# Kernel optimization log

Hardware: AMD Instinct MI355X
Metric: run time of the kernel (lower is better)

Reference implementation:

```python
import jax, jax.numpy as jnp
import numpy as np

N_REP = 8      # N: repeated gelu(LN(linear)) blocks
M_LAYERS = 4   # M: transformer encoder layers
SEQ = 100
D = 4
FF = 2048      # PyTorch TransformerEncoderLayer default dim_feedforward
H = 4          # nhead; head_dim = 1


def _ln(x, g, b, axes):
    m = jnp.mean(x, axis=axes, keepdims=True)
    v = jnp.var(x, axis=axes, keepdims=True)
    return (x - m) / jnp.sqrt(v + 1e-5) * g + b


def _encoder_layer(x, Win, bi, Wout, bout, W1, b1, W2, b2, g1, be1, g2, be2):
    # x: [S, Nb, D] with S = batch_size (batch_first=False!), Nb = 100
    S, Nb, E = x.shape
    qkv = x @ Win.T + bi                      # [S, Nb, 3D]
    q, k, v = jnp.split(qkv, 3, axis=-1)
    qh = q.reshape(S, Nb, H, E // H)          # head_dim = 1, scale 1/sqrt(1)=1
    kh = k.reshape(S, Nb, H, E // H)
    vh = v.reshape(S, Nb, H, E // H)
    scores = jnp.einsum('snhd,tnhd->nhst', qh, kh)   # [Nb, H, S, S]
    attn = jax.nn.softmax(scores, axis=-1)
    o = jnp.einsum('nhst,tnhd->snhd', attn, vh).reshape(S, Nb, E)
    o = o @ Wout.T + bout
    x = _ln(x + o, g1, be1, (-1,))            # post-norm (norm_first=False)
    f = jax.nn.relu(x @ W1.T + b1) @ W2.T + b2
    return _ln(x + f, g2, be2, (-1,))


def setup_inputs() -> dict:
    key = jax.random.key(0)
    ks = jax.random.split(key, 24)
    B = 256
    d = {}
    d['x'] = jax.random.normal(ks[0], (B, SEQ, D), dtype=jnp.float32)
    # conv1: kernel_size=1, 1->1 channel -> scalar affine
    d['conv_w'] = jax.random.normal(ks[1], (), dtype=jnp.float32) * 0.5 + 1.0
    d['conv_b'] = jax.random.normal(ks[2], (), dtype=jnp.float32) * 0.1
    # shared 4x4 linear (self.liner) and LayerNorm([100,4])
    d['Wl'] = jax.random.normal(ks[3], (D, D), dtype=jnp.float32) * 0.5
    d['bl'] = jax.random.normal(ks[4], (D,), dtype=jnp.float32) * 0.1
    d['ln_g'] = jnp.ones((SEQ, D), dtype=jnp.float32)
    d['ln_b'] = jnp.zeros((SEQ, D), dtype=jnp.float32)
    # transformer encoder params, stacked over M layers
    s = 0.3
    d['Win'] = jax.random.normal(ks[5], (M_LAYERS, 3 * D, D), dtype=jnp.float32) * s
    d['bi'] = jax.random.normal(ks[6], (M_LAYERS, 3 * D), dtype=jnp.float32) * 0.05
    d['Wout'] = jax.random.normal(ks[7], (M_LAYERS, D, D), dtype=jnp.float32) * s
    d['bout'] = jax.random.normal(ks[8], (M_LAYERS, D), dtype=jnp.float32) * 0.05
    d['W1'] = jax.random.normal(ks[9], (M_LAYERS, FF, D), dtype=jnp.float32) * 0.05
    d['b1'] = jax.random.normal(ks[10], (M_LAYERS, FF), dtype=jnp.float32) * 0.05
    d['W2'] = jax.random.normal(ks[11], (M_LAYERS, D, FF), dtype=jnp.float32) * 0.02
    d['b2'] = jax.random.normal(ks[12], (M_LAYERS, D), dtype=jnp.float32) * 0.05
    d['g1'] = jnp.ones((M_LAYERS, D), dtype=jnp.float32)
    d['be1'] = jnp.zeros((M_LAYERS, D), dtype=jnp.float32)
    d['g2'] = jnp.ones((M_LAYERS, D), dtype=jnp.float32)
    d['be2'] = jnp.zeros((M_LAYERS, D), dtype=jnp.float32)
    return d


def reference(x, conv_w, conv_b, Wl, bl, ln_g, ln_b,
              Win, bi, Wout, bout, W1, b1, W2, b2, g1, be1, g2, be2):
    # per-channel kernel_size=1 conv == elementwise affine (same scalar for all 4 channels)
    h = x * conv_w + conv_b                   # [B, 100, 4]
    for _ in range(N_REP):
        h = jax.nn.gelu(_ln(h @ Wl.T + bl, ln_g, ln_b, (-2, -1)), approximate=False)
    h = h @ Wl.T + bl
    for i in range(M_LAYERS):
        h = _encoder_layer(h, Win[i], bi[i], Wout[i], bout[i], W1[i], b1[i],
                           W2[i], b2[i], g1[i], be1[i], g2[i], be2[i])
    h = h @ Wl.T + bl
    return jax.nn.softmax(h, axis=2)
```

## Files before the change

### kernel.cpp

```cpp
#include <hip/hip_runtime.h>
#include <math.h>

#define SEQ   100
#define BATCH 256
#define NREP  8
#define FFD   2048
#define RSQRT2 0.70710678118654752440f

__device__ __forceinline__ float wsum(float v) {
#pragma unroll
  for (int o = 32; o > 0; o >>= 1) v += __shfl_xor(v, o, 64);
  return v;
}

__global__ __launch_bounds__(64) void k_stageA(
    const float* __restrict__ x, const float* __restrict__ convw,
    const float* __restrict__ convb, const float* __restrict__ Wl,
    const float* __restrict__ bl, const float* __restrict__ lng,
    const float* __restrict__ lnb, float* __restrict__ XT)
{
  const int b = blockIdx.x;
  const int lane = threadIdx.x;
  const bool act = lane < 50;

  const float cw = convw[0], cb = convb[0];
  float W[4][4], B[4];
#pragma unroll
  for (int j = 0; j < 4; ++j) {
    B[j] = bl[j];
#pragma unroll
    for (int d = 0; d < 4; ++d) W[j][d] = Wl[j * 4 + d];
  }

  float h[2][4] = {{0.f,0.f,0.f,0.f},{0.f,0.f,0.f,0.f}};
  float gg[2][4] = {{0.f}}, eb[2][4] = {{0.f}};
  if (act) {
#pragma unroll
    for (int p = 0; p < 2; ++p) {
      const int r = lane * 2 + p;
      float4 xr = *(const float4*)(x + (b * SEQ + r) * 4);
      h[p][0] = fmaf(xr.x, cw, cb); h[p][1] = fmaf(xr.y, cw, cb);
      h[p][2] = fmaf(xr.z, cw, cb); h[p][3] = fmaf(xr.w, cw, cb);
      float4 gv = *(const float4*)(lng + r * 4);
      float4 bv = *(const float4*)(lnb + r * 4);
      gg[p][0] = gv.x; gg[p][1] = gv.y; gg[p][2] = gv.z; gg[p][3] = gv.w;
      eb[p][0] = bv.x; eb[p][1] = bv.y; eb[p][2] = bv.z; eb[p][3] = bv.w;
    }
  }
  for (int it = 0; it < NREP; ++it) {
    float y[2][4] = {{0.f,0.f,0.f,0.f},{0.f,0.f,0.f,0.f}};
    float s1 = 0.f, s2 = 0.f;
    if (act) {
#pragma unroll
      for (int p = 0; p < 2; ++p)
#pragma unroll
        for (int j = 0; j < 4; ++j) {
          float yy = B[j];
#pragma unroll
          for (int d = 0; d < 4; ++d) yy = fmaf(h[p][d], W[j][d], yy);
          y[p][j] = yy; s1 += yy; s2 = fmaf(yy, yy, s2);
        }
    }
    s1 = wsum(s1); s2 = wsum(s2);
    const float mean = s1 * (1.0f / 400.0f);
    const float var  = s2 * (1.0f / 400.0f) - mean * mean;
    const float rstd = rsqrtf(var + 1e-5f);
    if (act) {
#pragma unroll
      for (int p = 0; p < 2; ++p)
#pragma unroll
        for (int j = 0; j < 4; ++j) {
          float vv = fmaf((y[p][j] - mean) * rstd, gg[p][j], eb[p][j]);
          h[p][j] = 0.5f * vv * (1.0f + erff(vv * RSQRT2));
        }
    }
  }
  if (act) {
#pragma unroll
    for (int p = 0; p < 2; ++p) {
      const int r = lane * 2 + p;
      float yy[4];
#pragma unroll
      for (int j = 0; j < 4; ++j) {
        float a = B[j];
#pragma unroll
        for (int d = 0; d < 4; ++d) a = fmaf(h[p][d], W[j][d], a);
        yy[j] = a;
      }
      *(float4*)(XT + (r * BATCH + b) * 4) =
          make_float4(yy[0], yy[1], yy[2], yy[3]);
    }
  }
}

__global__ __launch_bounds__(512) void k_layer(
    const float* __restrict__ XTin, float* __restrict__ XTout,
    const float* __restrict__ Wa,  const float* __restrict__ ba,
    const float* __restrict__ Wo,  const float* __restrict__ bo,
    const float* __restrict__ W1l, const float* __restrict__ b1l,
    const float* __restrict__ W2l, const float* __restrict__ b2l,
    const float* __restrict__ g1l, const float* __restrict__ e1l,
    const float* __restrict__ g2l, const float* __restrict__ e2l,
    const float* __restrict__ Wl,  const float* __restrict__ bl,
    float* __restrict__ out, const int last)
{
  const int n      = blockIdx.x;
  const int base_s = blockIdx.y * 128;
  const int t      = threadIdx.x;
  const int lane   = t & 63;
  const int wv     = t >> 6;
  const int h      = t >> 7;
  const int qr     = t & 127;

  __shared__ __align__(16) float wbuf[512][12];
  __shared__ float2 kv[4][256];
  __shared__ float  osm[4][128];
  __shared__ float  x1s[128][4];
  __shared__ float  pacc[8][128][4];
  __shared__ float  kred[8][2];

  float4 s_w1; float s_b1, s_w20, s_w21, s_w22, s_w23;
  {
    const int f = t;
    s_w1  = *(const float4*)(W1l + f * 4);
    s_b1  = b1l[f];
    s_w20 = W2l[f];           s_w21 = W2l[FFD + f];
    s_w22 = W2l[2 * FFD + f]; s_w23 = W2l[3 * FFD + f];
  }

  {
    const int s = t & 255, pr = t >> 8;
    float4 xr = *(const float4*)(XTin + (n * BATCH + s) * 4);
#pragma unroll
    for (int i = 0; i < 2; ++i) {
      const int hh = pr * 2 + i;
      const float* wk = Wa + (4 + hh) * 4;
      const float* wp = Wa + (8 + hh) * 4;
      float k = ba[4+hh] + xr.x*wk[0] + xr.y*wk[1] + xr.z*wk[2] + xr.w*wk[3];
      float v = ba[8+hh] + xr.x*wp[0] + xr.y*wp[1] + xr.z*wp[2] + xr.w*wp[3];
      kv[hh][s] = make_float2(k, v);
    }
  }
  float q;
  {
    float4 xr = *(const float4*)(XTin + (n * BATCH + base_s + qr) * 4);
    const float* wq = Wa + h * 4;
    q = ba[h] + xr.x*wq[0] + xr.y*wq[1] + xr.z*wq[2] + xr.w*wq[3];
  }
  __syncthreads();

  {
    float a = kv[h][qr].x, c = kv[h][qr + 128].x;
    float mx = fmaxf(a, c), mn = fminf(a, c);
#pragma unroll
    for (int o = 32; o > 0; o >>= 1) {
      mx = fmaxf(mx, __shfl_xor(mx, o, 64));
      mn = fminf(mn, __shfl_xor(mn, o, 64));
    }
    if (lane == 0) { kred[wv][0] = mx; kred[wv][1] = mn; }
  }
  __syncthreads();

  {
    const float kmx = fmaxf(kred[2*h][0], kred[2*h+1][0]);
    const float kmn = fminf(kred[2*h][1], kred[2*h+1][1]);
    const float m = (q >= 0.f) ? q * kmx : q * kmn;
    float d0=0.f,d1=0.f,d2=0.f,d3=0.f,n0=0.f,n1=0.f,n2=0.f,n3=0.f;
#pragma unroll 4
    for (int t2 = 0; t2 < 256; t2 += 8) {
      float4 a = *(const float4*)&kv[h][t2];
      float4 b = *(const float4*)&kv[h][t2+2];
      float4 c = *(const float4*)&kv[h][t2+4];
      float4 e = *(const float4*)&kv[h][t2+6];
      float p0 = __expf(fmaf(q, a.x, -m)); d0 += p0; n0 = fmaf(p0, a.y, n0);
      float p1 = __expf(fmaf(q, a.z, -m)); d1 += p1; n1 = fmaf(p1, a.w, n1);
      float p2 = __expf(fmaf(q, b.x, -m)); d2 += p2; n2 = fmaf(p2, b.y, n2);
      float p3 = __expf(fmaf(q, b.z, -m)); d3 += p3; n3 = fmaf(p3, b.w, n3);
      p0 = __expf(fmaf(q, c.x, -m)); d0 += p0; n0 = fmaf(p0, c.y, n0);
      p1 = __expf(fmaf(q, c.z, -m)); d1 += p1; n1 = fmaf(p1, c.w, n1);
      p2 = __expf(fmaf(q, e.x, -m)); d2 += p2; n2 = fmaf(p2, e.y, n2);
      p3 = __expf(fmaf(q, e.z, -m)); d3 += p3; n3 = fmaf(p3, e.w, n3);
    }
    osm[h][qr] = (n0+n1+n2+n3) / (d0+d1+d2+d3);
  }
  __syncthreads();

  {
    const int r = t >> 2, d = t & 3;
    const int g = n * BATCH + base_s + r;
    const float o0 = osm[0][r], o1 = osm[1][r], o2 = osm[2][r], o3 = osm[3][r];
    float rr = XTin[g * 4 + d] + bo[d]
             + o0 * Wo[d*4+0] + o1 * Wo[d*4+1] + o2 * Wo[d*4+2] + o3 * Wo[d*4+3];
    float sum = rr + __shfl_xor(rr, 1, 64); sum += __shfl_xor(sum, 2, 64);
    const float mean = 0.25f * sum;
    const float dv = rr - mean;
    float qq = dv * dv;
    float qs = qq + __shfl_xor(qq, 1, 64); qs += __shfl_xor(qs, 2, 64);
    const float rstd = rsqrtf(0.25f * qs + 1e-5f);
    x1s[r][d] = fmaf(dv * rstd, g1l[d], e1l[d]);
  }
  __syncthreads();

  const float xA0 = x1s[lane][0],    xA1 = x1s[lane][1];
  const float xA2 = x1s[lane][2],    xA3 = x1s[lane][3];
  const float xB0 = x1s[64+lane][0], xB1 = x1s[64+lane][1];
  const float xB2 = x1s[64+lane][2], xB3 = x1s[64+lane][3];
  float aA0=0.f,aA1=0.f,aA2=0.f,aA3=0.f;
  float aB0=0.f,aB1=0.f,aB2=0.f,aB3=0.f;

  for (int p = 0; p < 4; ++p) {
    __syncthreads();
    *(float4*)&wbuf[t][0] = s_w1;
    *(float4*)&wbuf[t][4] = make_float4(s_b1, s_w20, s_w21, s_w22);
    wbuf[t][8] = s_w23;
    if (p < 3) {
      const int f = (p + 1) * 512 + t;
      s_w1  = *(const float4*)(W1l + f * 4);
      s_b1  = b1l[f];
      s_w20 = W2l[f];           s_w21 = W2l[FFD + f];
      s_w22 = W2l[2 * FFD + f]; s_w23 = W2l[3 * FFD + f];
    }
    __syncthreads();
    const int fb = wv * 64;
#pragma unroll 4
    for (int j = 0; j < 64; ++j) {
      const int fl = fb + j;
      const float4 w1 = *(const float4*)&wbuf[fl][0];
      const float4 wb = *(const float4*)&wbuf[fl][4];
      const float w23 = wbuf[fl][8];
      float hA = fmaf(xA3, w1.w, fmaf(xA2, w1.z, fmaf(xA1, w1.y, fmaf(xA0, w1.x, wb.x))));
      hA = fmaxf(hA, 0.f);
      aA0 = fmaf(hA, wb.y, aA0); aA1 = fmaf(hA, wb.z, aA1);
      aA2 = fmaf(hA, wb.w, aA2); aA3 = fmaf(hA, w23, aA3);
      float hB = fmaf(xB3, w1.w, fmaf(xB2, w1.z, fmaf(xB1, w1.y, fmaf(xB0, w1.x, wb.x))));
      hB = fmaxf(hB, 0.f);
      aB0 = fmaf(hB, wb.y, aB0); aB1 = fmaf(hB, wb.z, aB1);
      aB2 = fmaf(hB, wb.w, aB2); aB3 = fmaf(hB, w23, aB3);
    }
  }
  *(float4*)&pacc[wv][lane][0]      = make_float4(aA0, aA1, aA2, aA3);
  *(float4*)&pacc[wv][64 + lane][0] = make_float4(aB0, aB1, aB2, aB3);
  __syncthreads();

  {
    const int r = t >> 2, d = t & 3;
    float s8 = b2l[d];
#pragma unroll
    for (int w = 0; w < 8; ++w) s8 += pacc[w][r][d];
    float val = x1s[r][d] + s8;
    float sum = val + __shfl_xor(val, 1, 64); sum += __shfl_xor(sum, 2, 64);
    const float mean = 0.25f * sum;
    const float dv = val - mean;
    float qq = dv * dv;
    float qs = qq + __shfl_xor(qq, 1, 64); qs += __shfl_xor(qs, 2, 64);
    const float rstd = rsqrtf(0.25f * qs + 1e-5f);
    const float res = fmaf(dv * rstd, g2l[d], e2l[d]);
    if (!last) XTout[(n * BATCH + base_s + r) * 4 + d] = res;
    else       x1s[r][d] = res;
  }

  if (last) {
    __syncthreads();
    const int r = t >> 2, j = t & 3;
    const float y = fmaf(x1s[r][3], Wl[j*4+3], fmaf(x1s[r][2], Wl[j*4+2],
                    fmaf(x1s[r][1], Wl[j*4+1], fmaf(x1s[r][0], Wl[j*4+0], bl[j]))));
    float mx = fmaxf(y, __shfl_xor(y, 1, 64)); mx = fmaxf(mx, __shfl_xor(mx, 2, 64));
    const float e = __expf(y - mx);
    float se = e + __shfl_xor(e, 1, 64); se += __shfl_xor(se, 2, 64);
    out[((base_s + r) * SEQ + n) * 4 + j] = e / se;
  }
}

extern "C" void kernel_launch(void* const* d_in, const int* in_sizes, int n_in,
                              void* d_out, int out_size, void* d_ws, size_t ws_size,
                              hipStream_t stream)
{
  const float* x     = (const float*)d_in[0];
  const float* convw = (const float*)d_in[1];
  const float* convb = (const float*)d_in[2];
  const float* Wl    = (const float*)d_in[3];
  const float* bl    = (const float*)d_in[4];
  const float* lng   = (const float*)d_in[5];
  const float* lnb   = (const float*)d_in[6];
  const float* Win   = (const float*)d_in[7];
  const float* bi    = (const float*)d_in[8];
  const float* Wout  = (const float*)d_in[9];
  const float* bout  = (const float*)d_in[10];
  const float* W1    = (const float*)d_in[11];
  const float* b1    = (const float*)d_in[12];
  const float* W2    = (const float*)d_in[13];
  const float* b2    = (const float*)d_in[14];
  const float* g1    = (const float*)d_in[15];
  const float* be1   = (const float*)d_in[16];
  const float* g2    = (const float*)d_in[17];
  const float* be2   = (const float*)d_in[18];

  float* XT0 = (float*)d_ws;
  float* XT1 = XT0 + SEQ * BATCH * 4;

  k_stageA<<<BATCH, 64, 0, stream>>>(x, convw, convb, Wl, bl, lng, lnb, XT0);
  for (int l = 0; l < 4; ++l) {
    const float* in  = (l & 1) ? XT1 : XT0;
    float*       outb= (l & 1) ? XT0 : XT1;
    k_layer<<<dim3(SEQ, 2), 512, 0, stream>>>(
        in, outb,
        Win + l * 48, bi + l * 12, Wout + l * 16, bout + l * 4,
        W1 + l * FFD * 4, b1 + l * FFD, W2 + l * 4 * FFD, b2 + l * 4,
        g1 + l * 4, be1 + l * 4, g2 + l * 4, be2 + l * 4,
        Wl, bl, (float*)d_out, (l == 3) ? 1 : 0);
  }
}
```

Measured before the change: 121.7 us.

## Split layer grid over FFN halves instead of sequence halves, defer LN2 to next layer

Each layer block now processes all 256 sequence rows but only half of the 2048 FFN features. Attention and LN1 are therefore computed redundantly in both blocks, while each FFN weight is loaded and reused across four row groups per thread. The two half-sum partials are written separately; the next layer (or a new final kernel) adds them and applies LN2. This removes the per-block weight streaming of all 2048 features and adds an extra partial buffer plus duplicated attention work.

```diff
diff --git a/kernel.cpp b/kernel.cpp
--- a/kernel.cpp
+++ b/kernel.cpp
@@ -5,6 +5,7 @@
 #define BATCH 256
 #define NREP  8
 #define FFD   2048
+#define COL   (SEQ * BATCH * 4)
 #define RSQRT2 0.70710678118654752440f
 
 __device__ __forceinline__ float wsum(float v) {
@@ -17,7 +18,7 @@
     const float* __restrict__ x, const float* __restrict__ convw,
     const float* __restrict__ convb, const float* __restrict__ Wl,
     const float* __restrict__ bl, const float* __restrict__ lng,
-    const float* __restrict__ lnb, float* __restrict__ XT)
+    const float* __restrict__ lnb, float* __restrict__ xG)
 {
   const int b = blockIdx.x;
   const int lane = threadIdx.x;
@@ -31,7 +32,6 @@
 #pragma unroll
     for (int d = 0; d < 4; ++d) W[j][d] = Wl[j * 4 + d];
   }
-
   float h[2][4] = {{0.f,0.f,0.f,0.f},{0.f,0.f,0.f,0.f}};
   float gg[2][4] = {{0.f}}, eb[2][4] = {{0.f}};
   if (act) {
@@ -87,70 +87,95 @@
         for (int d = 0; d < 4; ++d) a = fmaf(h[p][d], W[j][d], a);
         yy[j] = a;
       }
-      *(float4*)(XT + (r * BATCH + b) * 4) =
+      *(float4*)(xG + (r * BATCH + b) * 4) =
           make_float4(yy[0], yy[1], yy[2], yy[3]);
     }
   }
 }
 
 __global__ __launch_bounds__(512) void k_layer(
-    const float* __restrict__ XTin, float* __restrict__ XTout,
+    const float* __restrict__ in0, const float* __restrict__ in1,
+    const int first,
+    const float* __restrict__ g2p, const float* __restrict__ e2p,
+    float* __restrict__ vout,
     const float* __restrict__ Wa,  const float* __restrict__ ba,
     const float* __restrict__ Wo,  const float* __restrict__ bo,
     const float* __restrict__ W1l, const float* __restrict__ b1l,
     const float* __restrict__ W2l, const float* __restrict__ b2l,
-    const float* __restrict__ g1l, const float* __restrict__ e1l,
-    const float* __restrict__ g2l, const float* __restrict__ e2l,
-    const float* __restrict__ Wl,  const float* __restrict__ bl,
-    float* __restrict__ out, const int last)
+    const float* __restrict__ g1l, const float* __restrict__ e1l)
 {
-  const int n      = blockIdx.x;
-  const int base_s = blockIdx.y * 128;
-  const int t      = threadIdx.x;
-  const int lane   = t & 63;
-  const int wv     = t >> 6;
-  const int h      = t >> 7;
-  const int qr     = t & 127;
+  const int n    = blockIdx.x;
+  const int fh   = blockIdx.y;
+  const int t    = threadIdx.x;
+  const int lane = t & 63;
+  const int wv   = t >> 6;
+  const int h    = t >> 7;
+  const int qr0  = t & 127;
+  const int qr1  = qr0 + 128;
 
   __shared__ __align__(16) float wbuf[512][12];
   __shared__ float2 kv[4][256];
-  __shared__ float  osm[4][128];
-  __shared__ float  x1s[128][4];
-  __shared__ float  pacc[8][128][4];
+  __shared__ float  xs[256][4];
+  __shared__ float  x1s[256][4];
+  __shared__ float  osm[4][256];
+  __shared__ float  pacc[4][256][4];
   __shared__ float  kred[8][2];
 
+  const int fbase = fh * 1024;
   float4 s_w1; float s_b1, s_w20, s_w21, s_w22, s_w23;
   {
-    const int f = t;
+    const int f = fbase + t;
     s_w1  = *(const float4*)(W1l + f * 4);
     s_b1  = b1l[f];
     s_w20 = W2l[f];           s_w21 = W2l[FFD + f];
     s_w22 = W2l[2 * FFD + f]; s_w23 = W2l[3 * FFD + f];
   }
 
+  if (t < 256) {
+    if (first) {
+      float4 a = *(const float4*)(in0 + (n * BATCH + t) * 4);
+      xs[t][0] = a.x; xs[t][1] = a.y; xs[t][2] = a.z; xs[t][3] = a.w;
+    } else {
+      float4 a = *(const float4*)(in0 + (n * BATCH + t) * 4);
+      float4 b = *(const float4*)(in1 + (n * BATCH + t) * 4);
+      float v0 = a.x + b.x, v1 = a.y + b.y, v2 = a.z + b.z, v3 = a.w + b.w;
+      const float mean = 0.25f * (v0 + v1 + v2 + v3);
+      float d0 = v0-mean, d1 = v1-mean, d2 = v2-mean, d3 = v3-mean;
+      const float var = 0.25f * (d0*d0 + d1*d1 + d2*d2 + d3*d3);
+      const float rstd = rsqrtf(var + 1e-5f);
+      xs[t][0] = fmaf(d0 * rstd, g2p[0], e2p[0]);
+      xs[t][1] = fmaf(d1 * rstd, g2p[1], e2p[1]);
+      xs[t][2] = fmaf(d2 * rstd, g2p[2], e2p[2]);
+      xs[t][3] = fmaf(d3 * rstd, g2p[3], e2p[3]);
+    }
+  }
+  __syncthreads();
+
   {
     const int s = t & 255, pr = t >> 8;
-    float4 xr = *(const float4*)(XTin + (n * BATCH + s) * 4);
+    const float x0 = xs[s][0], x1 = xs[s][1], x2 = xs[s][2], x3 = xs[s][3];
 #pragma unroll
     for (int i = 0; i < 2; ++i) {
       const int hh = pr * 2 + i;
       const float* wk = Wa + (4 + hh) * 4;
       const float* wp = Wa + (8 + hh) * 4;
-      float k = ba[4+hh] + xr.x*wk[0] + xr.y*wk[1] + xr.z*wk[2] + xr.w*wk[3];
-      float v = ba[8+hh] + xr.x*wp[0] + xr.y*wp[1] + xr.z*wp[2] + xr.w*wp[3];
+      float k = ba[4+hh] + x0*wk[0] + x1*wk[1] + x2*wk[2] + x3*wk[3];
+      float v = ba[8+hh] + x0*wp[0] + x1*wp[1] + x2*wp[2] + x3*wp[3];
       kv[hh][s] = make_float2(k, v);
     }
   }
-  float q;
-  {
-    float4 xr = *(const float4*)(XTin + (n * BATCH + base_s + qr) * 4);
+  float q0, q1;
+  {
     const float* wq = Wa + h * 4;
-    q = ba[h] + xr.x*wq[0] + xr.y*wq[1] + xr.z*wq[2] + xr.w*wq[3];
-  }
-  __syncthreads();
-
-  {
-    float a = kv[h][qr].x, c = kv[h][qr + 128].x;
+    q0 = ba[h] + xs[qr0][0]*wq[0] + xs[qr0][1]*wq[1]
+               + xs[qr0][2]*wq[2] + xs[qr0][3]*wq[3];
+    q1 = ba[h] + xs[qr1][0]*wq[0] + xs[qr1][1]*wq[1]
+               + xs[qr1][2]*wq[2] + xs[qr1][3]*wq[3];
+  }
+  __syncthreads();
+
+  {
+    float a = kv[h][qr0].x, c = kv[h][qr1].x;
     float mx = fmaxf(a, c), mn = fminf(a, c);
 #pragma unroll
     for (int o = 32; o > 0; o >>= 1) {
@@ -164,111 +189,150 @@
   {
     const float kmx = fmaxf(kred[2*h][0], kred[2*h+1][0]);
     const float kmn = fminf(kred[2*h][1], kred[2*h+1][1]);
-    const float m = (q >= 0.f) ? q * kmx : q * kmn;
-    float d0=0.f,d1=0.f,d2=0.f,d3=0.f,n0=0.f,n1=0.f,n2=0.f,n3=0.f;
+    const float m0 = (q0 >= 0.f) ? q0 * kmx : q0 * kmn;
+    const float m1 = (q1 >= 0.f) ? q1 * kmx : q1 * kmn;
+    float dA0=0.f,dA1=0.f,nA0=0.f,nA1=0.f;
+    float dB0=0.f,dB1=0.f,nB0=0.f,nB1=0.f;
 #pragma unroll 4
-    for (int t2 = 0; t2 < 256; t2 += 8) {
-      float4 a = *(const float4*)&kv[h][t2];
-      float4 b = *(const float4*)&kv[h][t2+2];
-      float4 c = *(const float4*)&kv[h][t2+4];
-      float4 e = *(const float4*)&kv[h][t2+6];
-      float p0 = __expf(fmaf(q, a.x, -m)); d0 += p0; n0 = fmaf(p0, a.y, n0);
-      float p1 = __expf(fmaf(q, a.z, -m)); d1 += p1; n1 = fmaf(p1, a.w, n1);
-      float p2 = __expf(fmaf(q, b.x, -m)); d2 += p2; n2 = fmaf(p2, b.y, n2);
-      float p3 = __expf(fmaf(q, b.z, -m)); d3 += p3; n3 = fmaf(p3, b.w, n3);
-      p0 = __expf(fmaf(q, c.x, -m)); d0 += p0; n0 = fmaf(p0, c.y, n0);
-      p1 = __expf(fmaf(q, c.z, -m)); d1 += p1; n1 = fmaf(p1, c.w, n1);
-      p2 = __expf(fmaf(q, e.x, -m)); d2 += p2; n2 = fmaf(p2, e.y, n2);
-      p3 = __expf(fmaf(q, e.z, -m)); d3 += p3; n3 = fmaf(p3, e.w, n3);
-    }
-    osm[h][qr] = (n0+n1+n2+n3) / (d0+d1+d2+d3);
-  }
-  __syncthreads();
-
-  {
-    const int r = t >> 2, d = t & 3;
-    const int g = n * BATCH + base_s + r;
-    const float o0 = osm[0][r], o1 = osm[1][r], o2 = osm[2][r], o3 = osm[3][r];
-    float rr = XTin[g * 4 + d] + bo[d]
-             + o0 * Wo[d*4+0] + o1 * Wo[d*4+1] + o2 * Wo[d*4+2] + o3 * Wo[d*4+3];
-    float sum = rr + __shfl_xor(rr, 1, 64); sum += __shfl_xor(sum, 2, 64);
-    const float mean = 0.25f * sum;
-    const float dv = rr - mean;
-    float qq = dv * dv;
-    float qs = qq + __shfl_xor(qq, 1, 64); qs += __shfl_xor(qs, 2, 64);
-    const float rstd = rsqrtf(0.25f * qs + 1e-5f);
-    x1s[r][d] = fmaf(dv * rstd, g1l[d], e1l[d]);
-  }
-  __syncthreads();
-
-  const float xA0 = x1s[lane][0],    xA1 = x1s[lane][1];
-  const float xA2 = x1s[lane][2],    xA3 = x1s[lane][3];
-  const float xB0 = x1s[64+lane][0], xB1 = x1s[64+lane][1];
-  const float xB2 = x1s[64+lane][2], xB3 = x1s[64+lane][3];
-  float aA0=0.f,aA1=0.f,aA2=0.f,aA3=0.f;
-  float aB0=0.f,aB1=0.f,aB2=0.f,aB3=0.f;
-
-  for (int p = 0; p < 4; ++p) {
-    __syncthreads();
+    for (int t2 = 0; t2 < 256; t2 += 2) {
+      float4 kk = *(const float4*)&kv[h][t2];
+      float pA0 = __expf(fmaf(q0, kk.x, -m0));
+      float pA1 = __expf(fmaf(q0, kk.z, -m0));
+      float pB0 = __expf(fmaf(q1, kk.x, -m1));
+      float pB1 = __expf(fmaf(q1, kk.z, -m1));
+      dA0 += pA0; nA0 = fmaf(pA0, kk.y, nA0);
+      dA1 += pA1; nA1 = fmaf(pA1, kk.w, nA1);
+      dB0 += pB0; nB0 = fmaf(pB0, kk.y, nB0);
+      dB1 += pB1; nB1 = fmaf(pB1, kk.w, nB1);
+    }
+    osm[h][qr0] = (nA0 + nA1) / (dA0 + dA1);
+    osm[h][qr1] = (nB0 + nB1) / (dB0 + dB1);
+  }
+  __syncthreads();
+
+  if (t < 256) {
+    const float o0 = osm[0][t], o1 = osm[1][t], o2 = osm[2][t], o3 = osm[3][t];
+    float rr[4];
+#pragma unroll
+    for (int d = 0; d < 4; ++d)
+      rr[d] = xs[t][d] + bo[d] + o0*Wo[d*4+0] + o1*Wo[d*4+1]
+                               + o2*Wo[d*4+2] + o3*Wo[d*4+3];
+    const float mean = 0.25f * (rr[0] + rr[1] + rr[2] + rr[3]);
+    float d0 = rr[0]-mean, d1 = rr[1]-mean, d2 = rr[2]-mean, d3 = rr[3]-mean;
+    const float var = 0.25f * (d0*d0 + d1*d1 + d2*d2 + d3*d3);
+    const float rstd = rsqrtf(var + 1e-5f);
+    x1s[t][0] = fmaf(d0 * rstd, g1l[0], e1l[0]);
+    x1s[t][1] = fmaf(d1 * rstd, g1l[1], e1l[1]);
+    x1s[t][2] = fmaf(d2 * rstd, g1l[2], e1l[2]);
+    x1s[t][3] = fmaf(d3 * rstd, g1l[3], e1l[3]);
+  }
+  __syncthreads();
+
+  float xr[4][4];
+#pragma unroll
+  for (int rg = 0; rg < 4; ++rg) {
+    const int s = rg * 64 + lane;
+    xr[rg][0] = x1s[s][0]; xr[rg][1] = x1s[s][1];
+    xr[rg][2] = x1s[s][2]; xr[rg][3] = x1s[s][3];
+  }
+  float acc[4][4] = {{0.f,0.f,0.f,0.f},{0.f,0.f,0.f,0.f},
+                     {0.f,0.f,0.f,0.f},{0.f,0.f,0.f,0.f}};
+  for (int p = 0; p < 2; ++p) {
     *(float4*)&wbuf[t][0] = s_w1;
     *(float4*)&wbuf[t][4] = make_float4(s_b1, s_w20, s_w21, s_w22);
     wbuf[t][8] = s_w23;
-    if (p < 3) {
-      const int f = (p + 1) * 512 + t;
+    if (p == 0) {
+      const int f = fbase + 512 + t;
       s_w1  = *(const float4*)(W1l + f * 4);
       s_b1  = b1l[f];
       s_w20 = W2l[f];           s_w21 = W2l[FFD + f];
       s_w22 = W2l[2 * FFD + f]; s_w23 = W2l[3 * FFD + f];
     }
     __syncthreads();
-    const int fb = wv * 64;
+    const int fb = __builtin_amdgcn_readfirstlane(wv) * 64;
 #pragma unroll 4
     for (int j = 0; j < 64; ++j) {
       const int fl = fb + j;
       const float4 w1 = *(const float4*)&wbuf[fl][0];
       const float4 wb = *(const float4*)&wbuf[fl][4];
       const float w23 = wbuf[fl][8];
-      float hA = fmaf(xA3, w1.w, fmaf(xA2, w1.z, fmaf(xA1, w1.y, fmaf(xA0, w1.x, wb.x))));
-      hA = fmaxf(hA, 0.f);
-      aA0 = fmaf(hA, wb.y, aA0); aA1 = fmaf(hA, wb.z, aA1);
-      aA2 = fmaf(hA, wb.w, aA2); aA3 = fmaf(hA, w23, aA3);
-      float hB = fmaf(xB3, w1.w, fmaf(xB2, w1.z, fmaf(xB1, w1.y, fmaf(xB0, w1.x, wb.x))));
-      hB = fmaxf(hB, 0.f);
-      aB0 = fmaf(hB, wb.y, aB0); aB1 = fmaf(hB, wb.z, aB1);
-      aB2 = fmaf(hB, wb.w, aB2); aB3 = fmaf(hB, w23, aB3);
-    }
-  }
-  *(float4*)&pacc[wv][lane][0]      = make_float4(aA0, aA1, aA2, aA3);
-  *(float4*)&pacc[wv][64 + lane][0] = make_float4(aB0, aB1, aB2, aB3);
-  __syncthreads();
-
-  {
-    const int r = t >> 2, d = t & 3;
-    float s8 = b2l[d];
-#pragma unroll
-    for (int w = 0; w < 8; ++w) s8 += pacc[w][r][d];
-    float val = x1s[r][d] + s8;
-    float sum = val + __shfl_xor(val, 1, 64); sum += __shfl_xor(sum, 2, 64);
-    const float mean = 0.25f * sum;
-    const float dv = val - mean;
-    float qq = dv * dv;
-    float qs = qq + __shfl_xor(qq, 1, 64); qs += __shfl_xor(qs, 2, 64);
-    const float rstd = rsqrtf(0.25f * qs + 1e-5f);
-    const float res = fmaf(dv * rstd, g2l[d], e2l[d]);
-    if (!last) XTout[(n * BATCH + base_s + r) * 4 + d] = res;
-    else       x1s[r][d] = res;
-  }
-
-  if (last) {
+#pragma unroll
+      for (int rg = 0; rg < 4; ++rg) {
+        float hh = fmaf(xr[rg][3], w1.w, fmaf(xr[rg][2], w1.z,
+                   fmaf(xr[rg][1], w1.y, fmaf(xr[rg][0], w1.x, wb.x))));
+        hh = fmaxf(hh, 0.f);
+        acc[rg][0] = fmaf(hh, wb.y, acc[rg][0]);
+        acc[rg][1] = fmaf(hh, wb.z, acc[rg][1]);
+        acc[rg][2] = fmaf(hh, wb.w, acc[rg][2]);
+        acc[rg][3] = fmaf(hh, w23, acc[rg][3]);
+      }
+    }
     __syncthreads();
-    const int r = t >> 2, j = t & 3;
-    const float y = fmaf(x1s[r][3], Wl[j*4+3], fmaf(x1s[r][2], Wl[j*4+2],
-                    fmaf(x1s[r][1], Wl[j*4+1], fmaf(x1s[r][0], Wl[j*4+0], bl[j]))));
-    float mx = fmaxf(y, __shfl_xor(y, 1, 64)); mx = fmaxf(mx, __shfl_xor(mx, 2, 64));
-    const float e = __expf(y - mx);
-    float se = e + __shfl_xor(e, 1, 64); se += __shfl_xor(se, 2, 64);
-    out[((base_s + r) * SEQ + n) * 4 + j] = e / se;
-  }
+  }
+
+  if (wv < 4) {
+#pragma unroll
+    for (int rg = 0; rg < 4; ++rg)
+      *(float4*)&pacc[wv][rg * 64 + lane][0] =
+          make_float4(acc[rg][0], acc[rg][1], acc[rg][2], acc[rg][3]);
+  }
+  __syncthreads();
+  if (wv >= 4) {
+#pragma unroll
+    for (int rg = 0; rg < 4; ++rg) {
+      float4 o = *(float4*)&pacc[wv - 4][rg * 64 + lane][0];
+      o.x += acc[rg][0]; o.y += acc[rg][1];
+      o.z += acc[rg][2]; o.w += acc[rg][3];
+      *(float4*)&pacc[wv - 4][rg * 64 + lane][0] = o;
+    }
+  }
+  __syncthreads();
+
+  if (t < 256) {
+    float v[4];
+#pragma unroll
+    for (int d = 0; d < 4; ++d) {
+      float s4 = 0.5f * (x1s[t][d] + b2l[d]);
+#pragma unroll
+      for (int w = 0; w < 4; ++w) s4 += pacc[w][t][d];
+      v[d] = s4;
+    }
+    *(float4*)(vout + fh * COL + (n * BATCH + t) * 4) =
+        make_float4(v[0], v[1], v[2], v[3]);
+  }
+}
+
+__global__ __launch_bounds__(256) void k_fin(
+    const float* __restrict__ in0, const float* __restrict__ in1,
+    const float* __restrict__ g2p, const float* __restrict__ e2p,
+    const float* __restrict__ Wl,  const float* __restrict__ bl,
+    float* __restrict__ out)
+{
+  const int n = blockIdx.x, t = threadIdx.x;
+  float4 a = *(const float4*)(in0 + (n * BATCH + t) * 4);
+  float4 b = *(const float4*)(in1 + (n * BATCH + t) * 4);
+  float v0 = a.x + b.x, v1 = a.y + b.y, v2 = a.z + b.z, v3 = a.w + b.w;
+  const float mean = 0.25f * (v0 + v1 + v2 + v3);
+  float d0 = v0-mean, d1 = v1-mean, d2 = v2-mean, d3 = v3-mean;
+  const float var = 0.25f * (d0*d0 + d1*d1 + d2*d2 + d3*d3);
+  const float rstd = rsqrtf(var + 1e-5f);
+  float xf[4];
+  xf[0] = fmaf(d0 * rstd, g2p[0], e2p[0]);
+  xf[1] = fmaf(d1 * rstd, g2p[1], e2p[1]);
+  xf[2] = fmaf(d2 * rstd, g2p[2], e2p[2]);
+  xf[3] = fmaf(d3 * rstd, g2p[3], e2p[3]);
+  float y[4];
+#pragma unroll
+  for (int j = 0; j < 4; ++j)
+    y[j] = fmaf(xf[3], Wl[j*4+3], fmaf(xf[2], Wl[j*4+2],
+           fmaf(xf[1], Wl[j*4+1], fmaf(xf[0], Wl[j*4+0], bl[j]))));
+  float m = fmaxf(fmaxf(y[0], y[1]), fmaxf(y[2], y[3]));
+  float e[4], ssum = 0.f;
+#pragma unroll
+  for (int j = 0; j < 4; ++j) { e[j] = __expf(y[j] - m); ssum += e[j]; }
+  const float inv = 1.0f / ssum;
+  *(float4*)(out + (t * SEQ + n) * 4) =
+      make_float4(e[0]*inv, e[1]*inv, e[2]*inv, e[3]*inv);
 }
 
 extern "C" void kernel_launch(void* const* d_in, const int* in_sizes, int n_in,
@@ -295,18 +359,26 @@
   const float* g2    = (const float*)d_in[17];
   const float* be2   = (const float*)d_in[18];
 
-  float* XT0 = (float*)d_ws;
-  float* XT1 = XT0 + SEQ * BATCH * 4;
-
-  k_stageA<<<BATCH, 64, 0, stream>>>(x, convw, convb, Wl, bl, lng, lnb, XT0);
+  float* ws  = (float*)d_ws;
+  float* xG  = ws;
+  float* valA = ws + COL;
+  float* valB = ws + 3 * COL;
+
+  k_stageA<<<BATCH, 64, 0, stream>>>(x, convw, convb, Wl, bl, lng, lnb, xG);
+
   for (int l = 0; l < 4; ++l) {
-    const float* in  = (l & 1) ? XT1 : XT0;
-    float*       outb= (l & 1) ? XT0 : XT1;
+    float* cur        = (l & 1) ? valB : valA;
+    const float* prev = (l & 1) ? valA : valB;
+    const float* i0 = (l == 0) ? xG : prev;
+    const float* i1 = (l == 0) ? xG : prev + COL;
+    const int pl = (l == 0) ? 0 : l - 1;
     k_layer<<<dim3(SEQ, 2), 512, 0, stream>>>(
-        in, outb,
+        i0, i1, (l == 0) ? 1 : 0,
+        g2 + pl * 4, be2 + pl * 4, cur,
         Win + l * 48, bi + l * 12, Wout + l * 16, bout + l * 4,
         W1 + l * FFD * 4, b1 + l * FFD, W2 + l * 4 * FFD, b2 + l * 4,
-        g1 + l * 4, be1 + l * 4, g2 + l * 4, be2 + l * 4,
-        Wl, bl, (float*)d_out, (l == 3) ? 1 : 0);
-  }
-}
+        g1 + l * 4, be1 + l * 4);
+  }
+  k_fin<<<SEQ, 256, 0, stream>>>(valB, valB + COL, g2 + 12, be2 + 12,
+                                 Wl, bl, (float*)d_out);
+}
```

After: 133.6 us. 9.7% more time.

## Double k_layer block size to 1024 threads, splitting attention keys and FFN

Applied to the files above, without the earlier changes.

The per-layer kernel now launches 1024 threads per block instead of 512. Each attention query's key loop is split across two halves whose partial sums are merged in shared memory, and each wave processes 32 FFN hidden units instead of 64, with an extra shared-memory reduction pass. The intent is more waves in flight to hide LDS and exp latency in a grid of only 200 blocks. In exchange it adds synchronisation and reduction steps, and the launch bound of 1024 threads with a minimum-blocks hint of 4 may cap registers per thread.

```diff
diff --git a/kernel.cpp b/kernel.cpp
--- a/kernel.cpp
+++ b/kernel.cpp
@@ -31,7 +31,6 @@
 #pragma unroll
     for (int d = 0; d < 4; ++d) W[j][d] = Wl[j * 4 + d];
   }
-
   float h[2][4] = {{0.f,0.f,0.f,0.f},{0.f,0.f,0.f,0.f}};
   float gg[2][4] = {{0.f}}, eb[2][4] = {{0.f}};
   if (act) {
@@ -93,7 +92,7 @@
   }
 }
 
-__global__ __launch_bounds__(512) void k_layer(
+__global__ __launch_bounds__(1024, 4) void k_layer(
     const float* __restrict__ XTin, float* __restrict__ XTout,
     const float* __restrict__ Wa,  const float* __restrict__ ba,
     const float* __restrict__ Wo,  const float* __restrict__ bo,
@@ -109,18 +108,20 @@
   const int t      = threadIdx.x;
   const int lane   = t & 63;
   const int wv     = t >> 6;
-  const int h      = t >> 7;
+  const int h      = (t >> 7) & 3;
   const int qr     = t & 127;
+  const int kh     = t >> 9;
 
   __shared__ __align__(16) float wbuf[512][12];
   __shared__ float2 kv[4][256];
+  __shared__ float2 part[4][128][2];
   __shared__ float  osm[4][128];
   __shared__ float  x1s[128][4];
   __shared__ float  pacc[8][128][4];
-  __shared__ float  kred[8][2];
+  __shared__ float  kred[4][4][2];
 
   float4 s_w1; float s_b1, s_w20, s_w21, s_w22, s_w23;
-  {
+  if (t < 512) {
     const int f = t;
     s_w1  = *(const float4*)(W1l + f * 4);
     s_b1  = b1l[f];
@@ -129,17 +130,13 @@
   }
 
   {
-    const int s = t & 255, pr = t >> 8;
+    const int s = t & 255, hh = t >> 8;
     float4 xr = *(const float4*)(XTin + (n * BATCH + s) * 4);
-#pragma unroll
-    for (int i = 0; i < 2; ++i) {
-      const int hh = pr * 2 + i;
-      const float* wk = Wa + (4 + hh) * 4;
-      const float* wp = Wa + (8 + hh) * 4;
-      float k = ba[4+hh] + xr.x*wk[0] + xr.y*wk[1] + xr.z*wk[2] + xr.w*wk[3];
-      float v = ba[8+hh] + xr.x*wp[0] + xr.y*wp[1] + xr.z*wp[2] + xr.w*wp[3];
-      kv[hh][s] = make_float2(k, v);
-    }
+    const float* wk = Wa + (4 + hh) * 4;
+    const float* wp = Wa + (8 + hh) * 4;
+    float k = ba[4+hh] + xr.x*wk[0] + xr.y*wk[1] + xr.z*wk[2] + xr.w*wk[3];
+    float v = ba[8+hh] + xr.x*wp[0] + xr.y*wp[1] + xr.z*wp[2] + xr.w*wp[3];
+    kv[hh][s] = make_float2(k, v);
   }
   float q;
   {
@@ -150,47 +147,50 @@
   __syncthreads();
 
   {
-    float a = kv[h][qr].x, c = kv[h][qr + 128].x;
-    float mx = fmaxf(a, c), mn = fminf(a, c);
+    const int strip = (wv >> 3) * 2 + (wv & 1);
+    float k = kv[h][strip * 64 + lane].x;
+    float mx = k, mn = k;
 #pragma unroll
     for (int o = 32; o > 0; o >>= 1) {
       mx = fmaxf(mx, __shfl_xor(mx, o, 64));
       mn = fminf(mn, __shfl_xor(mn, o, 64));
     }
-    if (lane == 0) { kred[wv][0] = mx; kred[wv][1] = mn; }
+    if (lane == 0) { kred[h][strip][0] = mx; kred[h][strip][1] = mn; }
   }
   __syncthreads();
 
   {
-    const float kmx = fmaxf(kred[2*h][0], kred[2*h+1][0]);
-    const float kmn = fminf(kred[2*h][1], kred[2*h+1][1]);
+    const float kmx = fmaxf(fmaxf(kred[h][0][0], kred[h][1][0]),
+                            fmaxf(kred[h][2][0], kred[h][3][0]));
+    const float kmn = fminf(fminf(kred[h][0][1], kred[h][1][1]),
+                            fminf(kred[h][2][1], kred[h][3][1]));
     const float m = (q >= 0.f) ? q * kmx : q * kmn;
+    const int kb = kh * 128;
     float d0=0.f,d1=0.f,d2=0.f,d3=0.f,n0=0.f,n1=0.f,n2=0.f,n3=0.f;
 #pragma unroll 4
-    for (int t2 = 0; t2 < 256; t2 += 8) {
-      float4 a = *(const float4*)&kv[h][t2];
-      float4 b = *(const float4*)&kv[h][t2+2];
-      float4 c = *(const float4*)&kv[h][t2+4];
-      float4 e = *(const float4*)&kv[h][t2+6];
+    for (int i = 0; i < 128; i += 4) {
+      float4 a = *(const float4*)&kv[h][kb + i];
+      float4 b = *(const float4*)&kv[h][kb + i + 2];
       float p0 = __expf(fmaf(q, a.x, -m)); d0 += p0; n0 = fmaf(p0, a.y, n0);
       float p1 = __expf(fmaf(q, a.z, -m)); d1 += p1; n1 = fmaf(p1, a.w, n1);
       float p2 = __expf(fmaf(q, b.x, -m)); d2 += p2; n2 = fmaf(p2, b.y, n2);
       float p3 = __expf(fmaf(q, b.z, -m)); d3 += p3; n3 = fmaf(p3, b.w, n3);
-      p0 = __expf(fmaf(q, c.x, -m)); d0 += p0; n0 = fmaf(p0, c.y, n0);
-      p1 = __expf(fmaf(q, c.z, -m)); d1 += p1; n1 = fmaf(p1, c.w, n1);
-      p2 = __expf(fmaf(q, e.x, -m)); d2 += p2; n2 = fmaf(p2, e.y, n2);
-      p3 = __expf(fmaf(q, e.z, -m)); d3 += p3; n3 = fmaf(p3, e.w, n3);
-    }
-    osm[h][qr] = (n0+n1+n2+n3) / (d0+d1+d2+d3);
-  }
-  __syncthreads();
-
-  {
+    }
+    part[h][qr][kh] = make_float2(d0+d1+d2+d3, n0+n1+n2+n3);
+  }
+  __syncthreads();
+
+  if (t < 512) {
+    float4 pp = *(const float4*)&part[t >> 7][t & 127][0];
+    osm[t >> 7][t & 127] = (pp.y + pp.w) / (pp.x + pp.z);
+  }
+  __syncthreads();
+
+  if (t < 512) {
     const int r = t >> 2, d = t & 3;
-    const int g = n * BATCH + base_s + r;
     const float o0 = osm[0][r], o1 = osm[1][r], o2 = osm[2][r], o3 = osm[3][r];
-    float rr = XTin[g * 4 + d] + bo[d]
-             + o0 * Wo[d*4+0] + o1 * Wo[d*4+1] + o2 * Wo[d*4+2] + o3 * Wo[d*4+3];
+    float rr = XTin[(n * BATCH + base_s + r) * 4 + d] + bo[d]
+             + o0*Wo[d*4+0] + o1*Wo[d*4+1] + o2*Wo[d*4+2] + o3*Wo[d*4+3];
     float sum = rr + __shfl_xor(rr, 1, 64); sum += __shfl_xor(sum, 2, 64);
     const float mean = 0.25f * sum;
     const float dv = rr - mean;
@@ -209,21 +209,22 @@
   float aB0=0.f,aB1=0.f,aB2=0.f,aB3=0.f;
 
   for (int p = 0; p < 4; ++p) {
+    if (t < 512) {
+      *(float4*)&wbuf[t][0] = s_w1;
+      *(float4*)&wbuf[t][4] = make_float4(s_b1, s_w20, s_w21, s_w22);
+      wbuf[t][8] = s_w23;
+      if (p < 3) {
+        const int f = (p + 1) * 512 + t;
+        s_w1  = *(const float4*)(W1l + f * 4);
+        s_b1  = b1l[f];
+        s_w20 = W2l[f];           s_w21 = W2l[FFD + f];
+        s_w22 = W2l[2 * FFD + f]; s_w23 = W2l[3 * FFD + f];
+      }
+    }
     __syncthreads();
-    *(float4*)&wbuf[t][0] = s_w1;
-    *(float4*)&wbuf[t][4] = make_float4(s_b1, s_w20, s_w21, s_w22);
-    wbuf[t][8] = s_w23;
-    if (p < 3) {
-      const int f = (p + 1) * 512 + t;
-      s_w1  = *(const float4*)(W1l + f * 4);
-      s_b1  = b1l[f];
-      s_w20 = W2l[f];           s_w21 = W2l[FFD + f];
-      s_w22 = W2l[2 * FFD + f]; s_w23 = W2l[3 * FFD + f];
-    }
-    __syncthreads();
-    const int fb = wv * 64;
+    const int fb = __builtin_amdgcn_readfirstlane(wv) * 32;
 #pragma unroll 4
-    for (int j = 0; j < 64; ++j) {
+    for (int j = 0; j < 32; ++j) {
       const int fl = fb + j;
       const float4 w1 = *(const float4*)&wbuf[fl][0];
       const float4 wb = *(const float4*)&wbuf[fl][4];
@@ -237,12 +238,25 @@
       aB0 = fmaf(hB, wb.y, aB0); aB1 = fmaf(hB, wb.z, aB1);
       aB2 = fmaf(hB, wb.w, aB2); aB3 = fmaf(hB, w23, aB3);
     }
-  }
-  *(float4*)&pacc[wv][lane][0]      = make_float4(aA0, aA1, aA2, aA3);
-  *(float4*)&pacc[wv][64 + lane][0] = make_float4(aB0, aB1, aB2, aB3);
-  __syncthreads();
-
-  {
+    __syncthreads();
+  }
+
+  if (wv < 8) {
+    *(float4*)&pacc[wv][lane][0]      = make_float4(aA0, aA1, aA2, aA3);
+    *(float4*)&pacc[wv][64 + lane][0] = make_float4(aB0, aB1, aB2, aB3);
+  }
+  __syncthreads();
+  if (wv >= 8) {
+    float4 o = *(float4*)&pacc[wv - 8][lane][0];
+    o.x += aA0; o.y += aA1; o.z += aA2; o.w += aA3;
+    *(float4*)&pacc[wv - 8][lane][0] = o;
+    float4 o2 = *(float4*)&pacc[wv - 8][64 + lane][0];
+    o2.x += aB0; o2.y += aB1; o2.z += aB2; o2.w += aB3;
+    *(float4*)&pacc[wv - 8][64 + lane][0] = o2;
+  }
+  __syncthreads();
+
+  if (t < 512) {
     const int r = t >> 2, d = t & 3;
     float s8 = b2l[d];
 #pragma unroll
@@ -261,13 +275,15 @@
 
   if (last) {
     __syncthreads();
-    const int r = t >> 2, j = t & 3;
-    const float y = fmaf(x1s[r][3], Wl[j*4+3], fmaf(x1s[r][2], Wl[j*4+2],
-                    fmaf(x1s[r][1], Wl[j*4+1], fmaf(x1s[r][0], Wl[j*4+0], bl[j]))));
-    float mx = fmaxf(y, __shfl_xor(y, 1, 64)); mx = fmaxf(mx, __shfl_xor(mx, 2, 64));
-    const float e = __expf(y - mx);
-    float se = e + __shfl_xor(e, 1, 64); se += __shfl_xor(se, 2, 64);
-    out[((base_s + r) * SEQ + n) * 4 + j] = e / se;
+    if (t < 512) {
+      const int r = t >> 2, j = t & 3;
+      const float y = fmaf(x1s[r][3], Wl[j*4+3], fmaf(x1s[r][2], Wl[j*4+2],
+                      fmaf(x1s[r][1], Wl[j*4+1], fmaf(x1s[r][0], Wl[j*4+0], bl[j]))));
+      float mx = fmaxf(y, __shfl_xor(y, 1, 64)); mx = fmaxf(mx, __shfl_xor(mx, 2, 64));
+      const float e = __expf(y - mx);
+      float se = e + __shfl_xor(e, 1, 64); se += __shfl_xor(se, 2, 64);
+      out[((base_s + r) * SEQ + n) * 4 + j] = e / se;
+    }
   }
 }
 
@@ -302,7 +318,7 @@
   for (int l = 0; l < 4; ++l) {
     const float* in  = (l & 1) ? XT1 : XT0;
     float*       outb= (l & 1) ? XT0 : XT1;
-    k_layer<<<dim3(SEQ, 2), 512, 0, stream>>>(
+    k_layer<<<dim3(SEQ, 2), 1024, 0, stream>>>(
         in, outb,
         Win + l * 48, bi + l * 12, Wout + l * 16, bout + l * 4,
         W1 + l * FFD * 4, b1 + l * FFD, W2 + l * 4 * FFD, b2 + l * 4,
```

New measurement: 121.5 us. No clear change (-0.2%).
